# Optimization experiments

Measured on AMD Instinct MI355X. Metric: run time of the kernel, lower is better.

The kernel has to match this reference:

```python
import jax, jax.numpy as jnp
import numpy as np
import math

N_FUNC = 32
LR_START, LR_DECAY = 1.0, 0.977
WEIGHT_DECAY, AMP_DECAY, MM_LR = 0.01, 0.01, 0.03
N_SAMP, BATCH, MOMENTUM = 32, 16, 0.85
N_FEAT, N_TARGET, MEM_SIZE = 1024, 512, 16384
DATA_SIZE = 100
SQRT_NF = math.sqrt(N_FUNC)


def setup_inputs() -> dict:
    key = jax.random.key(0)
    ks = jax.random.split(key, 16)
    p = jnp.linspace(0.01, 0.99, N_FUNC)[:, None]
    center_freq = jnp.log(p / (1.0 - p))  # logit of linspace, as in __init__
    return {
        "t": DATA_SIZE,
        "data_size": DATA_SIZE,
        "ts": jax.random.randint(ks[0], (N_SAMP,), 0, DATA_SIZE + 1),
        "x": jax.random.normal(ks[1], (N_FEAT,), jnp.float32),
        "z": jax.random.normal(ks[2], (N_TARGET,), jnp.float32),
        "memory": jax.random.normal(ks[3], (MEM_SIZE, N_TARGET), jnp.float32),
        "t_memory": jax.random.randint(ks[4], (MEM_SIZE,), 0, DATA_SIZE),
        "feat_memory": jax.random.normal(ks[5], (MEM_SIZE, N_FEAT), jnp.float32),
        "amp_re": 1.0 / SQRT_NF + 0.01 * jax.random.normal(ks[6], (N_FUNC, N_TARGET), jnp.float32),
        "amp_im": 0.01 * jax.random.normal(ks[7], (N_FUNC, N_TARGET), jnp.float32),
        "freq": 0.1 * jax.random.normal(ks[8], (N_FUNC, 1), jnp.float32),
        "center_freq": center_freq.astype(jnp.float32),
        "res_proj": 0.02 * jax.random.normal(ks[9], (N_FEAT + N_TARGET, N_TARGET), jnp.float32),
        "feat_mean": 0.1 * jax.random.normal(ks[10], (N_FEAT,), jnp.float32),
        "bias": 0.1 * jax.random.normal(ks[11], (N_TARGET,), jnp.float32),
        "amp_grad_re": 0.01 * jax.random.normal(ks[12], (N_FUNC, N_TARGET), jnp.float32),
        "amp_grad_im": 0.01 * jax.random.normal(ks[13], (N_FUNC, N_TARGET), jnp.float32),
        "freq_grad": 0.01 * jax.random.normal(ks[14], (N_FUNC, 1), jnp.float32),
        "res_proj_grad": 0.001 * jax.random.normal(ks[15], (N_FEAT + N_TARGET, N_TARGET), jnp.float32),
    }


def _get_freq(freq, center_freq):
    fr = center_freq + jnp.tanh(freq) * (64.0 / N_FUNC)
    return jax.nn.sigmoid(fr) * 0.5


def _evaluate(t, amp_re, amp_im, freq, bias, center_freq):
    # t: [B]; amp: [F, T]; freq/center_freq: [F, 1]
    fr = _get_freq(freq, center_freq)                      # [F, 1]
    ph = (2.0 * math.pi) * t[:, None, None] * fr           # [B, F, 1]
    # Re(exp(i*ph) * (amp_re + i*amp_im)) = cos*amp_re - sin*amp_im
    z = (jnp.cos(ph) * amp_re - jnp.sin(ph) * amp_im).sum(1) / SQRT_NF
    return z + bias                                        # [B, T]


def _get_resid(x, z, res_proj, feat_mean, bias):
    r = jnp.concatenate([x - feat_mean, z - bias], axis=-1) @ res_proj
    return r / (jnp.abs(r) + 1.0)


def reference(t, data_size, ts, x, z, memory, t_memory, feat_memory,
              amp_re, amp_im, freq, center_freq, res_proj, feat_mean, bias,
              amp_grad_re, amp_grad_im, freq_grad, res_proj_grad):
    # scatter new sample into the ring buffers
    memory = memory.at[data_size].set(z)
    feat_memory = feat_memory.at[data_size].set(x)
    t_memory = t_memory.at[data_size].set(t)
    ds_new = data_size + 1
    lr = LR_START * LR_DECAY ** ds_new  # lr after this call's decay
    # running means (torch uses the already-incremented data_size)
    bias = (bias * ds_new + z) / (ds_new + 1)
    feat_mean = (feat_mean * ds_new + x) / (ds_new + 1)

    for b in range(N_SAMP // BATCH):
        batch = ts[b * BATCH:(b + 1) * BATCH]
        t_b = t_memory[batch].astype(jnp.float32)
        z_b = memory[batch]
        x_b = feat_memory[batch]

        def loss_fn(a_re, a_im, fq, rp):
            z_ = _evaluate(t_b, a_re, a_im, fq, bias, center_freq)
            amp_abs = jnp.sqrt(a_re ** 2 + a_im ** 2)
            loss = jnp.sqrt(amp_abs).sum() * AMP_DECAY
            loss = loss + jnp.abs(z_b - z_).sum(-1).mean()
            resid = _get_resid(x_b, z_, rp, feat_mean, bias)
            z2 = jax.lax.stop_gradient(z_) + resid
            res_loss = jnp.abs(z_b - z2).sum(-1).mean()
            # torch uses self.res_proj (buffer) here -> no grad through this term
            res_loss = res_loss + jnp.abs(jax.lax.stop_gradient(rp)).sum() * WEIGHT_DECAY
            return loss + res_loss * MM_LR

        ag_re, ag_im, fg, rg = jax.grad(loss_fn, argnums=(0, 1, 2, 3))(amp_re, amp_im, freq, res_proj)
        # momentum decay then normalized-grad accumulate, then SGD step
        anorm = jnp.sqrt((ag_re ** 2).sum() + (ag_im ** 2).sum()) + 1.0  # complex vector norm
        amp_grad_re = amp_grad_re * MOMENTUM + ag_re / anorm
        amp_grad_im = amp_grad_im * MOMENTUM + ag_im / anorm
        amp_re = amp_re - amp_grad_re * lr
        amp_im = amp_im - amp_grad_im * lr
        fnorm = jnp.sqrt((fg ** 2).sum()) + 1.0
        freq_grad = freq_grad * MOMENTUM + fg / fnorm
        freq = freq - freq_grad * lr
        rnorm = jnp.sqrt((rg ** 2).sum()) + 1.0
        res_proj_grad = res_proj_grad * MOMENTUM + rg / rnorm
        res_proj = res_proj - res_proj_grad * lr

    return (memory, t_memory, feat_memory, amp_re, amp_im, freq, res_proj,
            bias, feat_mean, amp_grad_re, amp_grad_im, freq_grad, res_proj_grad)
```

## Files before the change

### kernel.cpp

```cpp
#include <hip/hip_runtime.h>
#include <math.h>

#define NT 512
#define NF 1024
#define NFUNC 32
#define BATCHSZ 16

constexpr int O_MEM  = 0;
constexpr int O_TMEM = 8388608;
constexpr int O_FEAT = 8404992;
constexpr int O_ARE  = 25182208;
constexpr int O_AIM  = 25198592;
constexpr int O_FREQ = 25214976;
constexpr int O_RP   = 25215008;
constexpr int O_BIAS = 26001440;
constexpr int O_FM   = 26001952;
constexpr int O_AGR  = 26002976;
constexpr int O_AGI  = 26019360;
constexpr int O_FGR  = 26035744;
constexpr int O_RPG  = 26035776;

constexpr int W_LR    = 0;
constexpr int W_ANORM = 2;
constexpr int W_RNORM = 4;
constexpr int W_GFR   = 8;
constexpr int W_TB    = 72;
constexpr int W_C     = 96;
constexpr int W_S     = 608;
constexpr int W_CATZ  = 1120;
constexpr int W_CATX  = 9312;
constexpr int W_GR    = 25696;
constexpr int W_G     = 33888;
constexpr int W_AGRE  = 42080;
constexpr int W_AGIM  = 58464;
constexpr int W_RPART = 74848;

constexpr float MM_LR = 0.03f;
constexpr float AMP_DECAY = 0.01f;
constexpr float MOM = 0.85f;
constexpr float INV_SQRT_NF = 0.17677669529663687f;
constexpr float TWO_PI = 6.283185307179586f;

constexpr int NCOPY = 256;
constexpr long long U_TOTAL = 6295552LL;

__device__ __forceinline__ float sgnf(float x) {
    return (x > 0.f) ? 1.f : ((x < 0.f) ? -1.f : 0.f);
}

__device__ __forceinline__ float wave_reduce(float v) {
#pragma unroll
    for (int o = 32; o > 0; o >>= 1) v += __shfl_down(v, o, 64);
    return v;
}

__device__ __forceinline__ void copy_role(int rb, int cbase, int ccnt,
    const int* __restrict__ tptr, const int* __restrict__ dsptr,
    const float* __restrict__ x, const float* __restrict__ z,
    const float* __restrict__ memory, const int* __restrict__ t_memory,
    const float* __restrict__ feat_memory, float* __restrict__ out)
{
    const int dsv = *dsptr;
    const int tt  = *tptr;
    const int nthr = NCOPY * 256;
    for (int q = rb * 256 + (int)threadIdx.x; q * 4 < ccnt; q += nthr) {
#pragma unroll
        for (int w = 0; w < 4; ++w) {
            int rel = q * 4 + w;
            if (rel >= ccnt) break;
            int u = cbase + rel;
            if (u < 2097152) {
                int row = u >> 7;
                float4 v = (row == dsv) ? ((const float4*)z)[u & 127]
                                        : ((const float4*)memory)[u];
                ((float4*)(out + O_MEM))[u] = v;
            } else if (u < 6291456) {
                int f = u - 2097152;
                int row = f >> 8;
                float4 v = (row == dsv) ? ((const float4*)x)[f & 255]
                                        : ((const float4*)feat_memory)[f];
                ((float4*)(out + O_FEAT))[f] = v;
            } else {
                int f = u - 6291456;
                int4 iv = ((const int4*)t_memory)[f];
                int e = f * 4;
                float* o = out + O_TMEM + e;
                o[0] = (e + 0 == dsv) ? (float)tt : (float)iv.x;
                o[1] = (e + 1 == dsv) ? (float)tt : (float)iv.y;
                o[2] = (e + 2 == dsv) ? (float)tt : (float)iv.z;
                o[3] = (e + 3 == dsv) ? (float)tt : (float)iv.w;
            }
        }
    }
}

#define COPY_ARGS const int* __restrict__ tptr, const int* __restrict__ dsptr,            \
                  const float* __restrict__ x, const float* __restrict__ z,               \
                  const float* __restrict__ memory, const int* __restrict__ t_memory,     \
                  const float* __restrict__ feat_memory, int cbase, int ccnt
#define COPY_PASS tptr, dsptr, x, z, memory, t_memory, feat_memory

__global__ __launch_bounds__(256) void k_fwd_ab(int b, const int* __restrict__ ts,
    const float* __restrict__ cf,
    const float* __restrict__ are_src, const float* __restrict__ aim_src,
    const float* __restrict__ fq_src, const float* __restrict__ fm_in,
    const float* __restrict__ rp_src,
    float* __restrict__ out, float* __restrict__ ws, COPY_ARGS)
{
    const int bb = blockIdx.x, tid = threadIdx.x;
    if (bb >= 256) { copy_role(bb - 256, cbase, ccnt, COPY_PASS, out); return; }
    const int i = bb >> 4, s = bb & 15;
    __shared__ float c_l[32], s_l[32], cat[96];
    const int dsv = *dsptr;
    const int bi = ts[b * BATCHSZ + i];
    if (tid < 32) {
        float f  = fq_src[tid];
        float th = tanhf(f);
        float u  = cf[tid] + 2.f * th;
        float sg = 1.f / (1.f + expf(-u));
        float fr = 0.5f * sg;
        float tb = (bi == dsv) ? (float)(*tptr) : (float)t_memory[bi];
        float ph = TWO_PI * tb * fr;
        float cv = cosf(ph), sv = sinf(ph);
        c_l[tid] = cv; s_l[tid] = sv;
        if (s == 0) {
            ws[W_C + i*32 + tid] = cv; ws[W_S + i*32 + tid] = sv;
            if (tid == 0) ws[W_TB + i] = tb;
        }
    }
    if (bb == 0) {
        if (tid == 64) ws[W_ANORM + b] = 0.f;
        if (tid == 65) ws[W_RNORM + b] = 0.f;
        if (tid == 66 && b == 0) ws[W_LR] = (float)pow(0.977, (double)(dsv + 1));
        if (tid >= 96 && tid < 128) ws[W_GFR + b*32 + tid - 96] = 0.f;
    }
    __syncthreads();
    if (tid < 96) {
        int p = s * 96 + tid;
        float cv;
        if (p < NF) {
            const float nn = (float)(dsv + 1), dd = (float)(dsv + 2);
            float fmv = (fm_in[p] * nn + x[p]) / dd;
            float xv  = (bi == dsv) ? x[p] : feat_memory[bi*NF + p];
            cv = xv - fmv;
            ws[W_CATX + i*NF + p] = cv;
        } else {
            int q = p - NF;
            float acc = 0.f;
#pragma unroll
            for (int k = 0; k < 32; ++k)
                acc += c_l[k] * are_src[k*NT + q] - s_l[k] * aim_src[k*NT + q];
            cv = acc * INV_SQRT_NF;
            ws[W_CATZ + i*NT + q] = cv;
        }
        cat[tid] = cv;
    }
    __syncthreads();
    const int j = tid;
    const float* rpb = rp_src + (size_t)s * 96 * NT;
    float a0 = 0.f, a1 = 0.f, b0 = 0.f, b1 = 0.f;
#pragma unroll 8
    for (int p = 0; p < 96; p += 2) {
        float c0 = cat[p], c1 = cat[p + 1];
        a0 += c0 * rpb[p*NT + j];
        a1 += c0 * rpb[p*NT + j + 256];
        b0 += c1 * rpb[(p+1)*NT + j];
        b1 += c1 * rpb[(p+1)*NT + j + 256];
    }
    ws[W_RPART + s*8192 + i*NT + j]       = a0 + b0;
    ws[W_RPART + s*8192 + i*NT + j + 256] = a1 + b1;
}

__global__ __launch_bounds__(256) void k_eplg3(int b, const int* __restrict__ ts,
    const float* __restrict__ bias_in, const float* __restrict__ fm_in,
    const float* __restrict__ rp_src,
    float* __restrict__ out, float* __restrict__ ws, COPY_ARGS)
{
    const int bb = blockIdx.x, tid = threadIdx.x;
    if (bb >= 1024) { copy_role(bb - 1024, cbase, ccnt, COPY_PASS, out); return; }
    const int i = bb >> 6, jg = bb & 63;
    __shared__ float g_sh[NT], d_sh[NT];
    const int dsv = *dsptr;
    const int bi = ts[b * BATCHSZ + i];
    const float nn = (float)(dsv + 1), dd = (float)(dsv + 2);
#pragma unroll
    for (int ll = 0; ll < 2; ++ll) {
        int l = tid + ll * 256;
        float r = 0.f;
#pragma unroll
        for (int s = 0; s < 16; ++s) r += ws[W_RPART + s*8192 + i*NT + l];
        float bn = (bias_in[l] * nn + z[l]) / dd;
        float zj = ws[W_CATZ + i*NT + l] + bn;
        float zb = (bi == dsv) ? z[l] : memory[bi*NT + l];
        float s1 = sgnf(zj - zb);
        float ar = fabsf(r) + 1.f;
        float z2 = zj + r / ar;
        float g  = sgnf(z2 - zb) * (MM_LR / 16.f) / (ar * ar);
        g_sh[l] = g; d_sh[l] = s1 * (1.f / 16.f);
        if (jg == 0) {
            ws[W_GR + i*NT + l] = g;
            if (b == 0 && i == 0) out[O_BIAS + l] = bn;
        }
    }
    if (b == 0 && jg == 0 && i < 2) {
#pragma unroll
        for (int ll = 0; ll < 2; ++ll) {
            int p = i * 512 + tid + ll * 256;
            out[O_FM + p] = (fm_in[p] * nn + x[p]) / dd;
        }
    }
    __syncthreads();
    const int w = tid >> 6, lane = tid & 63;
#pragma unroll
    for (int jj = 0; jj < 2; ++jj) {
        int j = jg * 8 + w * 2 + jj;
        const float* rrow = rp_src + (size_t)(NF + j) * NT;
        float acc = 0.f;
#pragma unroll
        for (int l = lane; l < NT; l += 64) acc += g_sh[l] * rrow[l];
        acc = wave_reduce(acc);
        if (lane == 0) ws[W_G + i*NT + j] = d_sh[j] + acc;
    }
}

__global__ __launch_bounds__(256) void k_norms(int b,
    const float* __restrict__ are_src, const float* __restrict__ aim_src,
    float* __restrict__ out, float* __restrict__ ws, COPY_ARGS)
{
    __shared__ float red[4];
    const int bb = blockIdx.x, tid = threadIdx.x;
    if (bb >= 3264) { copy_role(bb - 3264, cbase, ccnt, COPY_PASS, out); return; }
    if (bb < 64) {
        int e = bb*256 + tid;
        int k = e >> 9;
        float gre = 0.f, gim = 0.f;
#pragma unroll
        for (int i2 = 0; i2 < 16; ++i2) {
            float G = ws[W_G + i2*NT + (e & 511)];
            gre += G * ws[W_C + i2*32 + k];
            gim += G * ws[W_S + i2*32 + k];
        }
        float re = are_src[e], im = aim_src[e];
        float aa = sqrtf(re*re + im*im);
        float dec = AMP_DECAY / (2.f * aa * sqrtf(aa));
        float agr =  gre * INV_SQRT_NF + re * dec;
        float agi = -gim * INV_SQRT_NF + im * dec;
        ws[W_AGRE + e] = agr;
        ws[W_AGIM + e] = agi;
        float v = wave_reduce(agr*agr + agi*agi);
        if ((tid & 63) == 0) red[tid >> 6] = v;
        __syncthreads();
        if (tid == 0) atomicAdd(&ws[W_ANORM + b], red[0]+red[1]+red[2]+red[3]);
    } else if (bb < 192) {
        int wid = tid >> 6, lane = tid & 63;
        int pair = (bb - 64)*4 + wid;
        int i = pair >> 5, k = pair & 31;
        float ck = ws[W_C + i*32 + k], sk = ws[W_S + i*32 + k];
        float acc = 0.f;
#pragma unroll
        for (int j = lane; j < NT; j += 64)
            acc += ws[W_G + i*NT + j] * (-sk * are_src[k*NT + j] - ck * aim_src[k*NT + j]);
        acc = wave_reduce(acc);
        if (lane == 0)
            atomicAdd(&ws[W_GFR + b*32 + k], acc * TWO_PI * ws[W_TB + i] * INV_SQRT_NF);
    } else {
        int e = (bb - 192)*256 + tid;
        int p = e >> 9, j = e & 511;
        float rg = 0.f;
#pragma unroll
        for (int i2 = 0; i2 < 16; ++i2) {
            float cat = (p < NF) ? ws[W_CATX + i2*NF + p]
                                 : ws[W_CATZ + i2*NT + (p - NF)];
            rg += cat * ws[W_GR + i2*NT + j];
        }
        float v = wave_reduce(rg * rg);
        if ((tid & 63) == 0) red[tid >> 6] = v;
        __syncthreads();
        if (tid == 0) atomicAdd(&ws[W_RNORM + b], red[0]+red[1]+red[2]+red[3]);
    }
}

__global__ __launch_bounds__(256) void k_upd(int b, const float* __restrict__ cf,
    const float* __restrict__ are_src, const float* __restrict__ aim_src,
    const float* __restrict__ agr_src, const float* __restrict__ agi_src,
    const float* __restrict__ fq_src,  const float* __restrict__ fgr_src,
    const float* __restrict__ rp_src,  const float* __restrict__ rpg_src,
    float* __restrict__ out, float* __restrict__ ws, COPY_ARGS)
{
    const int bb = blockIdx.x, tid = threadIdx.x;
    if (bb >= 3137) { copy_role(bb - 3137, cbase, ccnt, COPY_PASS, out); return; }
    const float lr = ws[W_LR];
    if (bb < 64) {
        int e = bb*256 + tid;
        float anorm = sqrtf(ws[W_ANORM + b]) + 1.f;
        float mr = agr_src[e]*MOM + ws[W_AGRE + e]/anorm;
        out[O_AGR + e] = mr; out[O_ARE + e] = are_src[e] - mr*lr;
        float mi = agi_src[e]*MOM + ws[W_AGIM + e]/anorm;
        out[O_AGI + e] = mi; out[O_AIM + e] = aim_src[e] - mi*lr;
    } else if (bb == 64) {
        if (tid < 64) {
            float fg = 0.f, th = 0.f;
            if (tid < 32) {
                float f = fq_src[tid];
                th = tanhf(f);
                float u  = cf[tid] + 2.f*th;
                float sg = 1.f / (1.f + expf(-u));
                fg = ws[W_GFR + b*32 + tid] * sg*(1.f-sg)*(1.f-th*th);
            }
            float t2 = fg*fg;
#pragma unroll
            for (int o = 32; o > 0; o >>= 1) t2 += __shfl_down(t2, o, 64);
            float tot = __shfl(t2, 0, 64);
            if (tid < 32) {
                float fnorm = sqrtf(tot) + 1.f;
                float m = fgr_src[tid]*MOM + fg/fnorm;
                out[O_FGR + tid] = m;
                out[O_FREQ + tid] = fq_src[tid] - m*lr;
            }
        }
    } else {
        int e = (bb - 65)*256 + tid;
        int p = e >> 9, j = e & 511;
        float rg = 0.f;
#pragma unroll
        for (int i2 = 0; i2 < 16; ++i2) {
            float cat = (p < NF) ? ws[W_CATX + i2*NF + p]
                                 : ws[W_CATZ + i2*NT + (p - NF)];
            rg += cat * ws[W_GR + i2*NT + j];
        }
        float rnorm = sqrtf(ws[W_RNORM + b]) + 1.f;
        float m = rpg_src[e]*MOM + rg/rnorm;
        out[O_RPG + e] = m; out[O_RP + e] = rp_src[e] - m*lr;
    }
}

extern "C" void kernel_launch(void* const* d_in, const int* in_sizes, int n_in,
                              void* d_out, int out_size, void* d_ws, size_t ws_size,
                              hipStream_t stream)
{
    const int*   t            = (const int*)d_in[0];
    const int*   dsp          = (const int*)d_in[1];
    const int*   ts           = (const int*)d_in[2];
    const float* x            = (const float*)d_in[3];
    const float* z            = (const float*)d_in[4];
    const float* memory       = (const float*)d_in[5];
    const int*   t_memory     = (const int*)d_in[6];
    const float* feat_memory  = (const float*)d_in[7];
    const float* amp_re       = (const float*)d_in[8];
    const float* amp_im       = (const float*)d_in[9];
    const float* freq         = (const float*)d_in[10];
    const float* cf           = (const float*)d_in[11];
    const float* res_proj     = (const float*)d_in[12];
    const float* feat_mean    = (const float*)d_in[13];
    const float* bias         = (const float*)d_in[14];
    const float* amp_grad_re  = (const float*)d_in[15];
    const float* amp_grad_im  = (const float*)d_in[16];
    const float* freq_grad    = (const float*)d_in[17];
    const float* res_proj_grad= (const float*)d_in[18];
    float* out = (float*)d_out;
    float* ws  = (float*)d_ws;

    const float* ARE[2] = { amp_re,        out + O_ARE };
    const float* AIM[2] = { amp_im,        out + O_AIM };
    const float* AGR[2] = { amp_grad_re,   out + O_AGR };
    const float* AGI[2] = { amp_grad_im,   out + O_AGI };
    const float* FQ [2] = { freq,          out + O_FREQ };
    const float* FGR[2] = { freq_grad,     out + O_FGR };
    const float* RP [2] = { res_proj,      out + O_RP };
    const float* RPG[2] = { res_proj_grad, out + O_RPG };

    const int per = 786944;
    int base = 0;
    auto nxt = [&](int& cb, int& cc) { cb = base; cc = per; base += cc; };
    int cb, cc;
    for (int b = 0; b < 2; ++b) {
        nxt(cb, cc);
        k_fwd_ab<<<256 + NCOPY, 256, 0, stream>>>(b, ts, cf, ARE[b], AIM[b], FQ[b],
            feat_mean, RP[b], out, ws, t, dsp, x, z, memory, t_memory, feat_memory, cb, cc);
        nxt(cb, cc);
        k_eplg3<<<1024 + NCOPY, 256, 0, stream>>>(b, ts, bias, feat_mean, RP[b], out, ws,
            t, dsp, x, z, memory, t_memory, feat_memory, cb, cc);
        nxt(cb, cc);
        k_norms<<<3264 + NCOPY, 256, 0, stream>>>(b, ARE[b], AIM[b], out, ws,
            t, dsp, x, z, memory, t_memory, feat_memory, cb, cc);
        nxt(cb, cc);
        k_upd<<<3137 + NCOPY, 256, 0, stream>>>(b, cf, ARE[b], AIM[b], AGR[b], AGI[b],
            FQ[b], FGR[b], RP[b], RPG[b], out, ws,
            t, dsp, x, z, memory, t_memory, feat_memory, cb, cc);
    }
}
```

Baseline: 360.7 us.

## Fuse eight stage kernels into one persistent kernel with grid barriers

Replaces the eight per-stage launches with a single persistent kernel of 256 blocks. Stages are separated by atomic-counter grid barriers kept in workspace, which is reset with a memset before the launch. The big memory copy is still split into slices, now run by every block inside each stage instead of by extra copy blocks. The work is remapped to the fixed grid: each block does more rows in the epilogue, and the norm stage uses grid-stride loops. This removes launch overhead and kernel tail gaps, but relies on all 256 blocks being resident at once and puts more serial work on each block.

```diff
diff --git a/kernel.cpp b/kernel.cpp
--- a/kernel.cpp
+++ b/kernel.cpp
@@ -3,7 +3,6 @@
 
 #define NT 512
 #define NF 1024
-#define NFUNC 32
 #define BATCHSZ 16
 
 constexpr int O_MEM  = 0;
@@ -25,6 +24,7 @@
 constexpr int W_RNORM = 4;
 constexpr int W_GFR   = 8;
 constexpr int W_TB    = 72;
+constexpr int W_BAR   = 88;
 constexpr int W_C     = 96;
 constexpr int W_S     = 608;
 constexpr int W_CATZ  = 1120;
@@ -41,8 +41,9 @@
 constexpr float INV_SQRT_NF = 0.17677669529663687f;
 constexpr float TWO_PI = 6.283185307179586f;
 
-constexpr int NCOPY = 256;
 constexpr long long U_TOTAL = 6295552LL;
+constexpr long long U_SLICE = 786944LL;
+constexpr int NB = 256;
 
 __device__ __forceinline__ float sgnf(float x) {
     return (x > 0.f) ? 1.f : ((x < 0.f) ? -1.f : 0.f);
@@ -54,283 +55,334 @@
     return v;
 }
 
-__device__ __forceinline__ void copy_role(int rb, int cbase, int ccnt,
-    const int* __restrict__ tptr, const int* __restrict__ dsptr,
+__device__ __forceinline__ void gbar(unsigned int* bar, int idx) {
+    __syncthreads();
+    if (threadIdx.x == 0) {
+        __threadfence();
+        atomicAdd(&bar[idx], 1u);
+        while (atomicAdd(&bar[idx], 0u) < (unsigned)NB)
+            __builtin_amdgcn_s_sleep(2);
+    }
+    __syncthreads();
+    __threadfence();
+}
+
+__device__ __forceinline__ float4 cp_fetch(long long u, int dsv, int tt,
+    const float* __restrict__ x, const float* __restrict__ z,
+    const float* __restrict__ memory, const int* __restrict__ t_memory,
+    const float* __restrict__ feat_memory, float* __restrict__ out,
+    float4** dstp)
+{
+    if (u < 2097152) {
+        int f = (int)u;
+        *dstp = (float4*)(out + O_MEM) + f;
+        return (f >> 7 == dsv) ? ((const float4*)z)[f & 127]
+                               : ((const float4*)memory)[f];
+    } else if (u < 6291456) {
+        int f = (int)(u - 2097152);
+        *dstp = (float4*)(out + O_FEAT) + f;
+        return (f >> 8 == dsv) ? ((const float4*)x)[f & 255]
+                               : ((const float4*)feat_memory)[f];
+    } else {
+        int f = (int)(u - 6291456);
+        *dstp = (float4*)(out + O_TMEM) + f;
+        int4 iv = ((const int4*)t_memory)[f];
+        int e = f * 4;
+        float4 v;
+        v.x = (e + 0 == dsv) ? (float)tt : (float)iv.x;
+        v.y = (e + 1 == dsv) ? (float)tt : (float)iv.y;
+        v.z = (e + 2 == dsv) ? (float)tt : (float)iv.z;
+        v.w = (e + 3 == dsv) ? (float)tt : (float)iv.w;
+        return v;
+    }
+}
+
+__device__ __forceinline__ void copy_units(long long ubase, long long uend,
+    int rank, int stride, int dsv, int tt,
     const float* __restrict__ x, const float* __restrict__ z,
     const float* __restrict__ memory, const int* __restrict__ t_memory,
     const float* __restrict__ feat_memory, float* __restrict__ out)
 {
-    const int dsv = *dsptr;
+    long long u = ubase + rank;
+    const long long s1 = stride, s2 = 2LL*stride, s3 = 3LL*stride, s4 = 4LL*stride;
+    for (; u + s3 < uend; u += s4) {
+        float4 *d0, *d1, *d2, *d3;
+        float4 v0 = cp_fetch(u,      dsv, tt, x, z, memory, t_memory, feat_memory, out, &d0);
+        float4 v1 = cp_fetch(u + s1, dsv, tt, x, z, memory, t_memory, feat_memory, out, &d1);
+        float4 v2 = cp_fetch(u + s2, dsv, tt, x, z, memory, t_memory, feat_memory, out, &d2);
+        float4 v3 = cp_fetch(u + s3, dsv, tt, x, z, memory, t_memory, feat_memory, out, &d3);
+        *d0 = v0; *d1 = v1; *d2 = v2; *d3 = v3;
+    }
+    for (; u < uend; u += s1) {
+        float4* d;
+        float4 v = cp_fetch(u, dsv, tt, x, z, memory, t_memory, feat_memory, out, &d);
+        *d = v;
+    }
+}
+
+__global__ __launch_bounds__(256) void k_all(
+    const int* __restrict__ tptr, const int* __restrict__ dsp,
+    const int* __restrict__ ts,
+    const float* __restrict__ x, const float* __restrict__ z,
+    const float* __restrict__ memory, const int* __restrict__ t_memory,
+    const float* __restrict__ feat_memory,
+    const float* __restrict__ amp_re, const float* __restrict__ amp_im,
+    const float* __restrict__ freq, const float* __restrict__ cf,
+    const float* __restrict__ res_proj, const float* __restrict__ feat_mean,
+    const float* __restrict__ bias,
+    const float* __restrict__ amp_grad_re, const float* __restrict__ amp_grad_im,
+    const float* __restrict__ freq_grad, const float* __restrict__ res_proj_grad,
+    float* __restrict__ out, float* __restrict__ ws)
+{
+    __shared__ float sh[1024];
+    unsigned int* bar = (unsigned int*)(ws + W_BAR);
+    const int bb = blockIdx.x, tid = threadIdx.x;
+    const int dsv = *dsp;
     const int tt  = *tptr;
-    const int nthr = NCOPY * 256;
-    for (int q = rb * 256 + (int)threadIdx.x; q * 4 < ccnt; q += nthr) {
-#pragma unroll
-        for (int w = 0; w < 4; ++w) {
-            int rel = q * 4 + w;
-            if (rel >= ccnt) break;
-            int u = cbase + rel;
-            if (u < 2097152) {
-                int row = u >> 7;
-                float4 v = (row == dsv) ? ((const float4*)z)[u & 127]
-                                        : ((const float4*)memory)[u];
-                ((float4*)(out + O_MEM))[u] = v;
-            } else if (u < 6291456) {
-                int f = u - 2097152;
-                int row = f >> 8;
-                float4 v = (row == dsv) ? ((const float4*)x)[f & 255]
-                                        : ((const float4*)feat_memory)[f];
-                ((float4*)(out + O_FEAT))[f] = v;
+    const float nn = (float)(dsv + 1), dd = (float)(dsv + 2);
+    const int crank = bb * 256 + tid;
+    const int cstride = NB * 256;
+
+    for (int b = 0; b < 2; ++b) {
+        const float* are_src = b ? out + O_ARE : amp_re;
+        const float* aim_src = b ? out + O_AIM : amp_im;
+        const float* agr_src = b ? out + O_AGR : amp_grad_re;
+        const float* agi_src = b ? out + O_AGI : amp_grad_im;
+        const float* fq_src  = b ? out + O_FREQ: freq;
+        const float* fgr_src = b ? out + O_FGR : freq_grad;
+        const float* rp_src  = b ? out + O_RP  : res_proj;
+        const float* rpg_src = b ? out + O_RPG : res_proj_grad;
+        const long long s_base = (long long)b * 4 * U_SLICE;
+        const int bix = b * 4;
+
+        {
+            const int i = bb >> 4, s = bb & 15;
+            float* c_l = sh;
+            float* s_l = sh + 32;
+            float* cat = sh + 64;
+            const int bi = ts[b * BATCHSZ + i];
+            if (tid < 32) {
+                float f  = fq_src[tid];
+                float th = tanhf(f);
+                float u  = cf[tid] + 2.f * th;
+                float sg = 1.f / (1.f + expf(-u));
+                float fr = 0.5f * sg;
+                float tb = (bi == dsv) ? (float)tt : (float)t_memory[bi];
+                float ph = TWO_PI * tb * fr;
+                float cv = cosf(ph), sv = sinf(ph);
+                c_l[tid] = cv; s_l[tid] = sv;
+                if (s == 0) {
+                    ws[W_C + i*32 + tid] = cv; ws[W_S + i*32 + tid] = sv;
+                    if (tid == 0) ws[W_TB + i] = tb;
+                }
+            }
+            if (bb == 0) {
+                if (tid == 64) ws[W_ANORM + b] = 0.f;
+                if (tid == 65) ws[W_RNORM + b] = 0.f;
+                if (tid == 66 && b == 0) ws[W_LR] = (float)pow(0.977, (double)(dsv + 1));
+                if (tid >= 96 && tid < 128) ws[W_GFR + b*32 + tid - 96] = 0.f;
+            }
+            __syncthreads();
+            if (tid < 96) {
+                int p = s * 96 + tid;
+                float cv;
+                if (p < NF) {
+                    float fmv = (feat_mean[p] * nn + x[p]) / dd;
+                    float xv  = (bi == dsv) ? x[p] : feat_memory[bi*NF + p];
+                    cv = xv - fmv;
+                    ws[W_CATX + i*NF + p] = cv;
+                } else {
+                    int q = p - NF;
+                    float acc = 0.f;
+#pragma unroll
+                    for (int k = 0; k < 32; ++k)
+                        acc += c_l[k] * are_src[k*NT + q] - s_l[k] * aim_src[k*NT + q];
+                    cv = acc * INV_SQRT_NF;
+                    ws[W_CATZ + i*NT + q] = cv;
+                }
+                cat[tid] = cv;
+            }
+            __syncthreads();
+            const int j = tid;
+            const float* rpb = rp_src + (size_t)s * 96 * NT;
+            float a0 = 0.f, a1 = 0.f, b0 = 0.f, b1 = 0.f;
+#pragma unroll 8
+            for (int p = 0; p < 96; p += 2) {
+                float c0 = cat[p], c1 = cat[p + 1];
+                a0 += c0 * rpb[p*NT + j];
+                a1 += c0 * rpb[p*NT + j + 256];
+                b0 += c1 * rpb[(p+1)*NT + j];
+                b1 += c1 * rpb[(p+1)*NT + j + 256];
+            }
+            ws[W_RPART + s*8192 + i*NT + j]       = a0 + b0;
+            ws[W_RPART + s*8192 + i*NT + j + 256] = a1 + b1;
+            copy_units(s_base, s_base + U_SLICE, crank, cstride,
+                       dsv, tt, x, z, memory, t_memory, feat_memory, out);
+        }
+        gbar(bar, bix + 0);
+
+        {
+            const int i = bb >> 4, jg = bb & 15;
+            float* g_sh = sh;
+            float* d_sh = sh + 512;
+            const int bi = ts[b * BATCHSZ + i];
+#pragma unroll
+            for (int ll = 0; ll < 2; ++ll) {
+                int l = tid + ll * 256;
+                float r = 0.f;
+#pragma unroll
+                for (int s = 0; s < 16; ++s) r += ws[W_RPART + s*8192 + i*NT + l];
+                float bn = (bias[l] * nn + z[l]) / dd;
+                float zj = ws[W_CATZ + i*NT + l] + bn;
+                float zb = (bi == dsv) ? z[l] : memory[bi*NT + l];
+                float s1 = sgnf(zj - zb);
+                float ar = fabsf(r) + 1.f;
+                float z2 = zj + r / ar;
+                float g  = sgnf(z2 - zb) * (MM_LR / 16.f) / (ar * ar);
+                g_sh[l] = g; d_sh[l] = s1 * (1.f / 16.f);
+                if (jg == 0) {
+                    ws[W_GR + i*NT + l] = g;
+                    if (b == 0 && i == 0) out[O_BIAS + l] = bn;
+                }
+            }
+            if (b == 0 && jg == 0 && i < 2) {
+#pragma unroll
+                for (int ll = 0; ll < 2; ++ll) {
+                    int p = i * 512 + tid + ll * 256;
+                    out[O_FM + p] = (feat_mean[p] * nn + x[p]) / dd;
+                }
+            }
+            __syncthreads();
+            const int w = tid >> 6, lane = tid & 63;
+            const float4* g4 = (const float4*)g_sh;
+#pragma unroll
+            for (int jj = 0; jj < 8; ++jj) {
+                int j = jg * 32 + w * 8 + jj;
+                const float4* rrow4 = (const float4*)(rp_src + (size_t)(NF + j) * NT);
+                float acc = 0.f;
+#pragma unroll
+                for (int k = 0; k < 2; ++k) {
+                    float4 a = rrow4[lane + 64*k];
+                    float4 g = g4[lane + 64*k];
+                    acc += a.x*g.x + a.y*g.y + a.z*g.z + a.w*g.w;
+                }
+                acc = wave_reduce(acc);
+                if (lane == 0) ws[W_G + i*NT + j] = d_sh[j] + acc;
+            }
+            copy_units(s_base + U_SLICE, s_base + 2*U_SLICE, crank, cstride,
+                       dsv, tt, x, z, memory, t_memory, feat_memory, out);
+        }
+        gbar(bar, bix + 1);
+
+        {
+            if (bb < 64) {
+                int e = bb*256 + tid;
+                int k = e >> 9;
+                float gre = 0.f, gim = 0.f;
+#pragma unroll
+                for (int i2 = 0; i2 < 16; ++i2) {
+                    float G = ws[W_G + i2*NT + (e & 511)];
+                    gre += G * ws[W_C + i2*32 + k];
+                    gim += G * ws[W_S + i2*32 + k];
+                }
+                float re = are_src[e], im = aim_src[e];
+                float aa = sqrtf(re*re + im*im);
+                float dec = AMP_DECAY / (2.f * aa * sqrtf(aa));
+                float agr =  gre * INV_SQRT_NF + re * dec;
+                float agi = -gim * INV_SQRT_NF + im * dec;
+                ws[W_AGRE + e] = agr;
+                ws[W_AGIM + e] = agi;
+                float v = wave_reduce(agr*agr + agi*agi);
+                if ((tid & 63) == 0) atomicAdd(&ws[W_ANORM + b], v);
+            } else if (bb < 96) {
+                int w = tid >> 6, lane = tid & 63;
+#pragma unroll
+                for (int q = 0; q < 4; ++q) {
+                    int pair = (bb - 64)*16 + w*4 + q;
+                    int i = pair >> 5, k = pair & 31;
+                    float ck = ws[W_C + i*32 + k], sk = ws[W_S + i*32 + k];
+                    float acc = 0.f;
+#pragma unroll
+                    for (int j = lane; j < NT; j += 64)
+                        acc += ws[W_G + i*NT + j] * (-sk * are_src[k*NT + j] - ck * aim_src[k*NT + j]);
+                    acc = wave_reduce(acc);
+                    if (lane == 0)
+                        atomicAdd(&ws[W_GFR + b*32 + k], acc * TWO_PI * ws[W_TB + i] * INV_SQRT_NF);
+                }
             } else {
-                int f = u - 6291456;
-                int4 iv = ((const int4*)t_memory)[f];
-                int e = f * 4;
-                float* o = out + O_TMEM + e;
-                o[0] = (e + 0 == dsv) ? (float)tt : (float)iv.x;
-                o[1] = (e + 1 == dsv) ? (float)tt : (float)iv.y;
-                o[2] = (e + 2 == dsv) ? (float)tt : (float)iv.z;
-                o[3] = (e + 3 == dsv) ? (float)tt : (float)iv.w;
-            }
+                const int rank3 = (bb - 96)*256 + tid;
+                const int stride3 = 160*256;
+                float v = 0.f;
+                for (int e = rank3; e < 786432; e += stride3) {
+                    int p = e >> 9, j = e & 511;
+                    float rg = 0.f;
+#pragma unroll
+                    for (int i2 = 0; i2 < 16; ++i2) {
+                        float cat = (p < NF) ? ws[W_CATX + i2*NF + p]
+                                             : ws[W_CATZ + i2*NT + (p - NF)];
+                        rg += cat * ws[W_GR + i2*NT + j];
+                    }
+                    v += rg * rg;
+                }
+                v = wave_reduce(v);
+                if ((tid & 63) == 0) atomicAdd(&ws[W_RNORM + b], v);
+            }
+            copy_units(s_base + 2*U_SLICE, s_base + 3*U_SLICE, crank, cstride,
+                       dsv, tt, x, z, memory, t_memory, feat_memory, out);
         }
-    }
-}
-
-#define COPY_ARGS const int* __restrict__ tptr, const int* __restrict__ dsptr,            \
-                  const float* __restrict__ x, const float* __restrict__ z,               \
-                  const float* __restrict__ memory, const int* __restrict__ t_memory,     \
-                  const float* __restrict__ feat_memory, int cbase, int ccnt
-#define COPY_PASS tptr, dsptr, x, z, memory, t_memory, feat_memory
-
-__global__ __launch_bounds__(256) void k_fwd_ab(int b, const int* __restrict__ ts,
-    const float* __restrict__ cf,
-    const float* __restrict__ are_src, const float* __restrict__ aim_src,
-    const float* __restrict__ fq_src, const float* __restrict__ fm_in,
-    const float* __restrict__ rp_src,
-    float* __restrict__ out, float* __restrict__ ws, COPY_ARGS)
-{
-    const int bb = blockIdx.x, tid = threadIdx.x;
-    if (bb >= 256) { copy_role(bb - 256, cbase, ccnt, COPY_PASS, out); return; }
-    const int i = bb >> 4, s = bb & 15;
-    __shared__ float c_l[32], s_l[32], cat[96];
-    const int dsv = *dsptr;
-    const int bi = ts[b * BATCHSZ + i];
-    if (tid < 32) {
-        float f  = fq_src[tid];
-        float th = tanhf(f);
-        float u  = cf[tid] + 2.f * th;
-        float sg = 1.f / (1.f + expf(-u));
-        float fr = 0.5f * sg;
-        float tb = (bi == dsv) ? (float)(*tptr) : (float)t_memory[bi];
-        float ph = TWO_PI * tb * fr;
-        float cv = cosf(ph), sv = sinf(ph);
-        c_l[tid] = cv; s_l[tid] = sv;
-        if (s == 0) {
-            ws[W_C + i*32 + tid] = cv; ws[W_S + i*32 + tid] = sv;
-            if (tid == 0) ws[W_TB + i] = tb;
+        gbar(bar, bix + 2);
+
+        {
+            const float lr = ws[W_LR];
+            if (bb < 64) {
+                int e = bb*256 + tid;
+                float anorm = sqrtf(ws[W_ANORM + b]) + 1.f;
+                float mr = agr_src[e]*MOM + ws[W_AGRE + e]/anorm;
+                out[O_AGR + e] = mr; out[O_ARE + e] = are_src[e] - mr*lr;
+                float mi = agi_src[e]*MOM + ws[W_AGIM + e]/anorm;
+                out[O_AGI + e] = mi; out[O_AIM + e] = aim_src[e] - mi*lr;
+            } else if (bb == 64) {
+                if (tid < 64) {
+                    float fg = 0.f, th = 0.f;
+                    if (tid < 32) {
+                        float f = fq_src[tid];
+                        th = tanhf(f);
+                        float u  = cf[tid] + 2.f*th;
+                        float sg = 1.f / (1.f + expf(-u));
+                        fg = ws[W_GFR + b*32 + tid] * sg*(1.f-sg)*(1.f-th*th);
+                    }
+                    float t2 = fg*fg;
+#pragma unroll
+                    for (int o = 32; o > 0; o >>= 1) t2 += __shfl_down(t2, o, 64);
+                    float tot = __shfl(t2, 0, 64);
+                    if (tid < 32) {
+                        float fnorm = sqrtf(tot) + 1.f;
+                        float m = fgr_src[tid]*MOM + fg/fnorm;
+                        out[O_FGR + tid] = m;
+                        out[O_FREQ + tid] = fq_src[tid] - m*lr;
+                    }
+                }
+            } else {
+                const int rank4 = (bb - 65)*256 + tid;
+                const int stride4 = 191*256;
+                float rnorm = sqrtf(ws[W_RNORM + b]) + 1.f;
+                for (int e = rank4; e < 786432; e += stride4) {
+                    int p = e >> 9, j = e & 511;
+                    float rg = 0.f;
+#pragma unroll
+                    for (int i2 = 0; i2 < 16; ++i2) {
+                        float cat = (p < NF) ? ws[W_CATX + i2*NF + p]
+                                             : ws[W_CATZ + i2*NT + (p - NF)];
+                        rg += cat * ws[W_GR + i2*NT + j];
+                    }
+                    float m = rpg_src[e]*MOM + rg/rnorm;
+                    out[O_RPG + e] = m; out[O_RP + e] = rp_src[e] - m*lr;
+                }
+            }
+            copy_units(s_base + 3*U_SLICE, s_base + 4*U_SLICE, crank, cstride,
+                       dsv, tt, x, z, memory, t_memory, feat_memory, out);
         }
-    }
-    if (bb == 0) {
-        if (tid == 64) ws[W_ANORM + b] = 0.f;
-        if (tid == 65) ws[W_RNORM + b] = 0.f;
-        if (tid == 66 && b == 0) ws[W_LR] = (float)pow(0.977, (double)(dsv + 1));
-        if (tid >= 96 && tid < 128) ws[W_GFR + b*32 + tid - 96] = 0.f;
-    }
-    __syncthreads();
-    if (tid < 96) {
-        int p = s * 96 + tid;
-        float cv;
-        if (p < NF) {
-            const float nn = (float)(dsv + 1), dd = (float)(dsv + 2);
-            float fmv = (fm_in[p] * nn + x[p]) / dd;
-            float xv  = (bi == dsv) ? x[p] : feat_memory[bi*NF + p];
-            cv = xv - fmv;
-            ws[W_CATX + i*NF + p] = cv;
-        } else {
-            int q = p - NF;
-            float acc = 0.f;
-#pragma unroll
-            for (int k = 0; k < 32; ++k)
-                acc += c_l[k] * are_src[k*NT + q] - s_l[k] * aim_src[k*NT + q];
-            cv = acc * INV_SQRT_NF;
-            ws[W_CATZ + i*NT + q] = cv;
-        }
-        cat[tid] = cv;
-    }
-    __syncthreads();
-    const int j = tid;
-    const float* rpb = rp_src + (size_t)s * 96 * NT;
-    float a0 = 0.f, a1 = 0.f, b0 = 0.f, b1 = 0.f;
-#pragma unroll 8
-    for (int p = 0; p < 96; p += 2) {
-        float c0 = cat[p], c1 = cat[p + 1];
-        a0 += c0 * rpb[p*NT + j];
-        a1 += c0 * rpb[p*NT + j + 256];
-        b0 += c1 * rpb[(p+1)*NT + j];
-        b1 += c1 * rpb[(p+1)*NT + j + 256];
-    }
-    ws[W_RPART + s*8192 + i*NT + j]       = a0 + b0;
-    ws[W_RPART + s*8192 + i*NT + j + 256] = a1 + b1;
-}
-
-__global__ __launch_bounds__(256) void k_eplg3(int b, const int* __restrict__ ts,
-    const float* __restrict__ bias_in, const float* __restrict__ fm_in,
-    const float* __restrict__ rp_src,
-    float* __restrict__ out, float* __restrict__ ws, COPY_ARGS)
-{
-    const int bb = blockIdx.x, tid = threadIdx.x;
-    if (bb >= 1024) { copy_role(bb - 1024, cbase, ccnt, COPY_PASS, out); return; }
-    const int i = bb >> 6, jg = bb & 63;
-    __shared__ float g_sh[NT], d_sh[NT];
-    const int dsv = *dsptr;
-    const int bi = ts[b * BATCHSZ + i];
-    const float nn = (float)(dsv + 1), dd = (float)(dsv + 2);
-#pragma unroll
-    for (int ll = 0; ll < 2; ++ll) {
-        int l = tid + ll * 256;
-        float r = 0.f;
-#pragma unroll
-        for (int s = 0; s < 16; ++s) r += ws[W_RPART + s*8192 + i*NT + l];
-        float bn = (bias_in[l] * nn + z[l]) / dd;
-        float zj = ws[W_CATZ + i*NT + l] + bn;
-        float zb = (bi == dsv) ? z[l] : memory[bi*NT + l];
-        float s1 = sgnf(zj - zb);
-        float ar = fabsf(r) + 1.f;
-        float z2 = zj + r / ar;
-        float g  = sgnf(z2 - zb) * (MM_LR / 16.f) / (ar * ar);
-        g_sh[l] = g; d_sh[l] = s1 * (1.f / 16.f);
-        if (jg == 0) {
-            ws[W_GR + i*NT + l] = g;
-            if (b == 0 && i == 0) out[O_BIAS + l] = bn;
-        }
-    }
-    if (b == 0 && jg == 0 && i < 2) {
-#pragma unroll
-        for (int ll = 0; ll < 2; ++ll) {
-            int p = i * 512 + tid + ll * 256;
-            out[O_FM + p] = (fm_in[p] * nn + x[p]) / dd;
-        }
-    }
-    __syncthreads();
-    const int w = tid >> 6, lane = tid & 63;
-#pragma unroll
-    for (int jj = 0; jj < 2; ++jj) {
-        int j = jg * 8 + w * 2 + jj;
-        const float* rrow = rp_src + (size_t)(NF + j) * NT;
-        float acc = 0.f;
-#pragma unroll
-        for (int l = lane; l < NT; l += 64) acc += g_sh[l] * rrow[l];
-        acc = wave_reduce(acc);
-        if (lane == 0) ws[W_G + i*NT + j] = d_sh[j] + acc;
-    }
-}
-
-__global__ __launch_bounds__(256) void k_norms(int b,
-    const float* __restrict__ are_src, const float* __restrict__ aim_src,
-    float* __restrict__ out, float* __restrict__ ws, COPY_ARGS)
-{
-    __shared__ float red[4];
-    const int bb = blockIdx.x, tid = threadIdx.x;
-    if (bb >= 3264) { copy_role(bb - 3264, cbase, ccnt, COPY_PASS, out); return; }
-    if (bb < 64) {
-        int e = bb*256 + tid;
-        int k = e >> 9;
-        float gre = 0.f, gim = 0.f;
-#pragma unroll
-        for (int i2 = 0; i2 < 16; ++i2) {
-            float G = ws[W_G + i2*NT + (e & 511)];
-            gre += G * ws[W_C + i2*32 + k];
-            gim += G * ws[W_S + i2*32 + k];
-        }
-        float re = are_src[e], im = aim_src[e];
-        float aa = sqrtf(re*re + im*im);
-        float dec = AMP_DECAY / (2.f * aa * sqrtf(aa));
-        float agr =  gre * INV_SQRT_NF + re * dec;
-        float agi = -gim * INV_SQRT_NF + im * dec;
-        ws[W_AGRE + e] = agr;
-        ws[W_AGIM + e] = agi;
-        float v = wave_reduce(agr*agr + agi*agi);
-        if ((tid & 63) == 0) red[tid >> 6] = v;
-        __syncthreads();
-        if (tid == 0) atomicAdd(&ws[W_ANORM + b], red[0]+red[1]+red[2]+red[3]);
-    } else if (bb < 192) {
-        int wid = tid >> 6, lane = tid & 63;
-        int pair = (bb - 64)*4 + wid;
-        int i = pair >> 5, k = pair & 31;
-        float ck = ws[W_C + i*32 + k], sk = ws[W_S + i*32 + k];
-        float acc = 0.f;
-#pragma unroll
-        for (int j = lane; j < NT; j += 64)
-            acc += ws[W_G + i*NT + j] * (-sk * are_src[k*NT + j] - ck * aim_src[k*NT + j]);
-        acc = wave_reduce(acc);
-        if (lane == 0)
-            atomicAdd(&ws[W_GFR + b*32 + k], acc * TWO_PI * ws[W_TB + i] * INV_SQRT_NF);
-    } else {
-        int e = (bb - 192)*256 + tid;
-        int p = e >> 9, j = e & 511;
-        float rg = 0.f;
-#pragma unroll
-        for (int i2 = 0; i2 < 16; ++i2) {
-            float cat = (p < NF) ? ws[W_CATX + i2*NF + p]
-                                 : ws[W_CATZ + i2*NT + (p - NF)];
-            rg += cat * ws[W_GR + i2*NT + j];
-        }
-        float v = wave_reduce(rg * rg);
-        if ((tid & 63) == 0) red[tid >> 6] = v;
-        __syncthreads();
-        if (tid == 0) atomicAdd(&ws[W_RNORM + b], red[0]+red[1]+red[2]+red[3]);
-    }
-}
-
-__global__ __launch_bounds__(256) void k_upd(int b, const float* __restrict__ cf,
-    const float* __restrict__ are_src, const float* __restrict__ aim_src,
-    const float* __restrict__ agr_src, const float* __restrict__ agi_src,
-    const float* __restrict__ fq_src,  const float* __restrict__ fgr_src,
-    const float* __restrict__ rp_src,  const float* __restrict__ rpg_src,
-    float* __restrict__ out, float* __restrict__ ws, COPY_ARGS)
-{
-    const int bb = blockIdx.x, tid = threadIdx.x;
-    if (bb >= 3137) { copy_role(bb - 3137, cbase, ccnt, COPY_PASS, out); return; }
-    const float lr = ws[W_LR];
-    if (bb < 64) {
-        int e = bb*256 + tid;
-        float anorm = sqrtf(ws[W_ANORM + b]) + 1.f;
-        float mr = agr_src[e]*MOM + ws[W_AGRE + e]/anorm;
-        out[O_AGR + e] = mr; out[O_ARE + e] = are_src[e] - mr*lr;
-        float mi = agi_src[e]*MOM + ws[W_AGIM + e]/anorm;
-        out[O_AGI + e] = mi; out[O_AIM + e] = aim_src[e] - mi*lr;
-    } else if (bb == 64) {
-        if (tid < 64) {
-            float fg = 0.f, th = 0.f;
-            if (tid < 32) {
-                float f = fq_src[tid];
-                th = tanhf(f);
-                float u  = cf[tid] + 2.f*th;
-                float sg = 1.f / (1.f + expf(-u));
-                fg = ws[W_GFR + b*32 + tid] * sg*(1.f-sg)*(1.f-th*th);
-            }
-            float t2 = fg*fg;
-#pragma unroll
-            for (int o = 32; o > 0; o >>= 1) t2 += __shfl_down(t2, o, 64);
-            float tot = __shfl(t2, 0, 64);
-            if (tid < 32) {
-                float fnorm = sqrtf(tot) + 1.f;
-                float m = fgr_src[tid]*MOM + fg/fnorm;
-                out[O_FGR + tid] = m;
-                out[O_FREQ + tid] = fq_src[tid] - m*lr;
-            }
-        }
-    } else {
-        int e = (bb - 65)*256 + tid;
-        int p = e >> 9, j = e & 511;
-        float rg = 0.f;
-#pragma unroll
-        for (int i2 = 0; i2 < 16; ++i2) {
-            float cat = (p < NF) ? ws[W_CATX + i2*NF + p]
-                                 : ws[W_CATZ + i2*NT + (p - NF)];
-            rg += cat * ws[W_GR + i2*NT + j];
-        }
-        float rnorm = sqrtf(ws[W_RNORM + b]) + 1.f;
-        float m = rpg_src[e]*MOM + rg/rnorm;
-        out[O_RPG + e] = m; out[O_RP + e] = rp_src[e] - m*lr;
+        if (b == 0) gbar(bar, bix + 3);
     }
 }
 
@@ -360,32 +412,10 @@
     float* out = (float*)d_out;
     float* ws  = (float*)d_ws;
 
-    const float* ARE[2] = { amp_re,        out + O_ARE };
-    const float* AIM[2] = { amp_im,        out + O_AIM };
-    const float* AGR[2] = { amp_grad_re,   out + O_AGR };
-    const float* AGI[2] = { amp_grad_im,   out + O_AGI };
-    const float* FQ [2] = { freq,          out + O_FREQ };
-    const float* FGR[2] = { freq_grad,     out + O_FGR };
-    const float* RP [2] = { res_proj,      out + O_RP };
-    const float* RPG[2] = { res_proj_grad, out + O_RPG };
-
-    const int per = 786944;
-    int base = 0;
-    auto nxt = [&](int& cb, int& cc) { cb = base; cc = per; base += cc; };
-    int cb, cc;
-    for (int b = 0; b < 2; ++b) {
-        nxt(cb, cc);
-        k_fwd_ab<<<256 + NCOPY, 256, 0, stream>>>(b, ts, cf, ARE[b], AIM[b], FQ[b],
-            feat_mean, RP[b], out, ws, t, dsp, x, z, memory, t_memory, feat_memory, cb, cc);
-        nxt(cb, cc);
-        k_eplg3<<<1024 + NCOPY, 256, 0, stream>>>(b, ts, bias, feat_mean, RP[b], out, ws,
-            t, dsp, x, z, memory, t_memory, feat_memory, cb, cc);
-        nxt(cb, cc);
-        k_norms<<<3264 + NCOPY, 256, 0, stream>>>(b, ARE[b], AIM[b], out, ws,
-            t, dsp, x, z, memory, t_memory, feat_memory, cb, cc);
-        nxt(cb, cc);
-        k_upd<<<3137 + NCOPY, 256, 0, stream>>>(b, cf, ARE[b], AIM[b], AGR[b], AGI[b],
-            FQ[b], FGR[b], RP[b], RPG[b], out, ws,
-            t, dsp, x, z, memory, t_memory, feat_memory, cb, cc);
-    }
-}
+    hipMemsetAsync((char*)d_ws + W_BAR * sizeof(float), 0, 8 * sizeof(unsigned int), stream);
+
+    k_all<<<NB, 256, 0, stream>>>(t, dsp, ts, x, z, memory, t_memory, feat_memory,
+                                  amp_re, amp_im, freq, cf, res_proj, feat_mean, bias,
+                                  amp_grad_re, amp_grad_im, freq_grad, res_proj_grad,
+                                  out, ws);
+}
```

After: 739.1 us. 105% more time.
